# Kernel tuning notes

Hardware: AMD Instinct MI355X
Metric: run time of the kernel (lower is better)

## Reference

```python
import jax, jax.numpy as jnp
import numpy as np

B, K, V = 8192, 1024, 2


def setup_inputs() -> dict:
    key = jax.random.key(0)
    k1, k2, k3, k4, k5, k6 = jax.random.split(key, 6)
    z = jax.random.normal(k1, (B, K), dtype=jnp.float32)
    # -1 means no intervention for that sample
    intervention_target = jax.random.randint(k2, (B,), -1, K)
    intervention_variant = jax.random.randint(k3, (B,), 0, V)
    raw_adjacency = jax.random.normal(k4, (K, K), dtype=jnp.float32) * 0.05
    intervention_means = jax.random.normal(k5, (K, V), dtype=jnp.float32)
    intervention_log_scales = jax.random.normal(k6, (K, V), dtype=jnp.float32) * 0.1
    return {
        "z": z,
        "intervention_target": intervention_target,
        "intervention_variant": intervention_variant,
        "raw_adjacency": raw_adjacency,
        "intervention_means": intervention_means,
        "intervention_log_scales": intervention_log_scales,
    }


def _scm_forward(z, target, variant, raw_adjacency, means, log_scales):
    Kd = z.shape[1]
    # strictly-lower-triangular adjacency (row j holds parents of node j)
    A = raw_adjacency * jnp.tril(jnp.ones((Kd, Kd), z.dtype), k=-1)

    def step(u, xs):
        a_row, mean_row, logsc_row, z_j, j = xs
        # forward substitution: u_j = z_j + sum_{i<j} A[j,i] * u_i
        # columns >= j of u are still zero and A row is zero there too
        value = z_j + u @ a_row  # [B]
        # intervention overwrite for samples with target == j
        m = mean_row[variant]                 # [B]
        s = jnp.exp(logsc_row[variant])       # [B]
        value = jnp.where(target == j, m + s * z_j, value)
        u = jax.lax.dynamic_update_slice(u, value[:, None], (0, j))
        return u, None

    u0 = jnp.zeros_like(z)
    xs = (A, means, log_scales, z.T, jnp.arange(Kd))
    u, _ = jax.lax.scan(step, u0, xs)
    return u


def reference(z, intervention_target, intervention_variant, raw_adjacency,
              intervention_means, intervention_log_scales):
    return _scm_forward(z, intervention_target, intervention_variant,
                        raw_adjacency, intervention_means, intervention_log_scales)
```

## Files before the change

### kernel.cpp

```cpp
#include <hip/hip_runtime.h>
#include <hip/hip_bf16.h>
#include <cstdint>

#define KDIM 1024
#define BDIM 8192
#define VDIM 2
#define NBLK 16

typedef __attribute__((ext_vector_type(8))) short short8;
typedef __attribute__((ext_vector_type(4))) float f32x4;

__device__ inline unsigned short f2bf(float x) {
  unsigned u = __builtin_bit_cast(unsigned, x);
  u = (u + 0x7FFFu + ((u >> 16) & 1u)) >> 16;
  return (unsigned short)u;
}

__device__ inline float bf2f(unsigned short x) {
  return __builtin_bit_cast(float, (unsigned)x << 16);
}


#define STAGE_T(DST, SRC, ROW0, COL0, LD)                                   \
  {                                                                         \
    const float* _s = (SRC);                                                \
    _Pragma("unroll") for (int _p = 0; _p < 4; ++_p) {                      \
      const int _m = _p * 16 + rw;                                          \
      float4 _v = *(const float4*)(_s + (size_t)((ROW0) + _m) * (LD) +      \
                                   (COL0) + 4 * k4);                        \
      (DST)[4 * k4 + 0][_m] = _v.x;                                         \
      (DST)[4 * k4 + 1][_m] = _v.y;                                         \
      (DST)[4 * k4 + 2][_m] = _v.z;                                         \
      (DST)[4 * k4 + 3][_m] = _v.w;                                         \
    }                                                                       \
  }

#define STAGE_D(DST, SRC, ROW0, COL0, LD)                                   \
  {                                                                         \
    const float* _s = (SRC);                                                \
    _Pragma("unroll") for (int _p = 0; _p < 4; ++_p) {                      \
      const int _kk = _p * 16 + rw;                                         \
      *(float4*)&(DST)[_kk][4 * k4] =                                       \
          *(const float4*)(_s + (size_t)((ROW0) + _kk) * (LD) + (COL0) +    \
                           4 * k4);                                         \
    }                                                                       \
  }

#define ZERO_ACC                                                            \
  _Pragma("unroll") for (int _a = 0; _a < 4; ++_a)                          \
      _Pragma("unroll") for (int _b = 0; _b < 4; ++_b) acc[_a][_b] = 0.f;

__device__ __forceinline__ void mac64(const float (*Ls)[68],
                                      const float (*Rs)[68], int tm, int tn,
                                      float acc[4][4]) {
#pragma unroll 4
  for (int k = 0; k < 64; ++k) {
    const float4 av = *(const float4*)&Ls[k][4 * tm];
    const float4 bv = *(const float4*)&Rs[k][4 * tn];
    const float aa[4] = {av.x, av.y, av.z, av.w};
    const float bb4[4] = {bv.x, bv.y, bv.z, bv.w};
#pragma unroll
    for (int a = 0; a < 4; ++a)
#pragma unroll
      for (int b = 0; b < 4; ++b) acc[a][b] += aa[a] * bb4[b];
  }
}

#define STORE_MT(R0, C0)                                                    \
  _Pragma("unroll") for (int _a = 0; _a < 4; ++_a) {                        \
    *(float4*)(MT + (size_t)((R0) + 4 * tm + _a) * KDIM + (C0) + 4 * tn) =  \
        make_float4(acc[_a][0], acc[_a][1], acc[_a][2], acc[_a][3]);        \
  }

#define MBF_TILE(R0, C0, BUF)                                               \
  {                                                                         \
    __syncthreads();                                                        \
    _Pragma("unroll") for (int _a = 0; _a < 4; ++_a)                        \
        _Pragma("unroll") for (int _b = 0; _b < 4; ++_b)                    \
            (BUF)[4 * tm + _a][4 * tn + _b] = acc[_a][_b];                  \
    __syncthreads();                                                        \
    const int _tr = tid >> 4, _tc = tid & 15;                               \
    _Pragma("unroll") for (int _p = 0; _p < 4; ++_p) {                      \
      const int _il = _p * 16 + _tr;                                        \
      ushort4 _o;                                                           \
      _o.x = f2bf((BUF)[4 * _tc + 0][_il]);                                 \
      _o.y = f2bf((BUF)[4 * _tc + 1][_il]);                                 \
      _o.z = f2bf((BUF)[4 * _tc + 2][_il]);                                 \
      _o.w = f2bf((BUF)[4 * _tc + 3][_il]);                                 \
      *(ushort4*)(Mbf + (size_t)((C0) + _il) * KDIM + (R0) + 4 * _tc) = _o; \
    }                                                                       \
  }

__global__ __launch_bounds__(256) void prep_inv(const float* __restrict__ A,
                                                float* __restrict__ MT,
                                                unsigned short* __restrict__ Mbf) {
  __shared__ float As[64 * 64];
  const int base = blockIdx.x * 64;
  for (int i = threadIdx.x; i < 64 * 64; i += 256)
    As[i] = A[(size_t)(base + (i >> 6)) * KDIM + base + (i & 63)];
  __syncthreads();
  if (threadIdx.x < 64) {
    const int c = threadIdx.x;
    float m[64];
#pragma unroll
    for (int r = 0; r < 64; ++r) m[r] = (r == c) ? 1.f : 0.f;
#pragma unroll
    for (int r = 1; r < 64; ++r) {
      float acc0 = 0.f, acc1 = 0.f;
#pragma unroll
      for (int i = 0; i < 64; ++i) {
        if (i >= r) break;
        if (i & 1) acc1 += As[r * 64 + i] * m[i];
        else       acc0 += As[r * 64 + i] * m[i];
      }
      const float v = acc0 + acc1;
      m[r] = (r > c) ? v : m[r];
    }
#pragma unroll
    for (int r = 0; r < 64; r += 4) {
      float4 v = make_float4(m[r], m[r + 1], m[r + 2], m[r + 3]);
      *(float4*)(MT + (size_t)(base + c) * KDIM + base + r) = v;
    }
#pragma unroll
    for (int r = 0; r < 64; ++r)
      Mbf[(size_t)(base + r) * KDIM + base + c] = f2bf(m[r]);
  }
}

__global__ __launch_bounds__(256) void comb01(const float* __restrict__ A,
                                              float* __restrict__ MT,
                                              unsigned short* __restrict__ Mbf) {
  int b = blockIdx.x;
  const int rt = b & 1;
  const int jt = (b >> 1) & 1;
  const int s = b >> 2;
  const int base = s * 256;

  __shared__ float Ls[64][68];
  __shared__ float Rs[64][68];
  __shared__ float tQ0L[64][68];
  __shared__ float tQ0H[64][68];
  __shared__ float tP0[64][68];
  __shared__ float tP1[64][68];

  const int tid = threadIdx.x;
  const int k4 = tid & 15;
  const int rw = tid >> 4;
  const int tm = tid >> 4;
  const int tn = tid & 15;
  float acc[4][4];

  if (jt == 0) {
    STAGE_T(Ls, MT, base, base, KDIM);
    STAGE_T(Rs, A, base + 64, base, KDIM);
    __syncthreads();
    ZERO_ACC;
    mac64(Ls, Rs, tm, tn, acc);
    __syncthreads();
#pragma unroll
    for (int a = 0; a < 4; ++a)
#pragma unroll
      for (int b2 = 0; b2 < 4; ++b2) tP0[4 * tn + b2][4 * tm + a] = acc[a][b2];
    STAGE_D(Rs, MT, base + 64, base + 64, KDIM);
    __syncthreads();
    ZERO_ACC;
    mac64(tP0, Rs, tm, tn, acc);
    __syncthreads();
#pragma unroll
    for (int a = 0; a < 4; ++a)
#pragma unroll
      for (int b2 = 0; b2 < 4; ++b2) tQ0L[4 * tn + b2][4 * tm + a] = acc[a][b2];
    if (rt == 0) {
      STORE_MT(base, base + 64);
      MBF_TILE(base, base + 64, Rs);
    }
  }
  __syncthreads();

  if (rt == 1) {
    STAGE_T(Ls, MT, base + 128, base + 128, KDIM);
    STAGE_T(Rs, A, base + 192, base + 128, KDIM);
    __syncthreads();
    ZERO_ACC;
    mac64(Ls, Rs, tm, tn, acc);
    __syncthreads();
#pragma unroll
    for (int a = 0; a < 4; ++a)
#pragma unroll
      for (int b2 = 0; b2 < 4; ++b2) tP1[4 * tn + b2][4 * tm + a] = acc[a][b2];
    STAGE_D(Rs, MT, base + 192, base + 192, KDIM);
    __syncthreads();
    ZERO_ACC;
    mac64(tP1, Rs, tm, tn, acc);
    __syncthreads();
#pragma unroll
    for (int a = 0; a < 4; ++a)
#pragma unroll
      for (int b2 = 0; b2 < 4; ++b2) tQ0H[4 * tm + a][4 * tn + b2] = acc[a][b2];
    if (jt == 1) {
      STORE_MT(base + 128, base + 192);
      MBF_TILE(base + 128, base + 192, Rs);
    }
  }
  __syncthreads();

  STAGE_T(Ls, MT, base + 64 * jt, base + 64 * jt, KDIM);
  __syncthreads();
  for (int kb2 = 0; kb2 <= rt; ++kb2) {
    ZERO_ACC;
    for (int kb = jt; kb < 2; ++kb) {
      STAGE_T(Rs, A, base + 128 + 64 * kb2, base + 64 * kb, KDIM);
      __syncthreads();
      mac64(kb == jt ? Ls : tQ0L, Rs, tm, tn, acc);
      __syncthreads();
    }
    if (kb2 == 0) {
#pragma unroll
      for (int a = 0; a < 4; ++a)
#pragma unroll
        for (int b2 = 0; b2 < 4; ++b2) tP0[4 * tn + b2][4 * tm + a] = acc[a][b2];
    } else {
#pragma unroll
      for (int a = 0; a < 4; ++a)
#pragma unroll
        for (int b2 = 0; b2 < 4; ++b2) tP1[4 * tn + b2][4 * tm + a] = acc[a][b2];
    }
  }
  __syncthreads();

  ZERO_ACC;
  if (rt == 0) {
    STAGE_D(Rs, MT, base + 128, base + 128, KDIM);
    __syncthreads();
    mac64(tP0, Rs, tm, tn, acc);
    __syncthreads();
  } else {
    mac64(tP0, tQ0H, tm, tn, acc);
    __syncthreads();
    STAGE_D(Rs, MT, base + 192, base + 192, KDIM);
    __syncthreads();
    mac64(tP1, Rs, tm, tn, acc);
    __syncthreads();
  }
  STORE_MT(base + 64 * jt, base + 128 + 64 * rt);
  MBF_TILE(base + 64 * jt, base + 128 + 64 * rt, Rs);
}

__global__ __launch_bounds__(256) void p4_stream(
    const float* __restrict__ A, float* __restrict__ MT,
    float* __restrict__ Pt, const float* __restrict__ Z,
    unsigned short* __restrict__ Zbf, unsigned short* __restrict__ Mbf,
    int do_zbf) {
  __shared__ float Ls[64][68];
  __shared__ float Rs[64][68];

  if (blockIdx.x >= 32) {
    const int wid = blockIdx.x - 32;
    const int nw = gridDim.x - 32;
    const int idx0 = wid * 256 + threadIdx.x;
    const int stride = nw * 256;
    const float4 z4 = make_float4(0.f, 0.f, 0.f, 0.f);
    const uint4 u4 = make_uint4(0u, 0u, 0u, 0u);

    for (int i = idx0; i < 256 * 1024; i += stride) {
      const int blk = i >> 10, off = i & 1023;
      const int bi = blk >> 4, bj = blk & 15;
      if (bi <= bj) continue;
      *(float4*)(MT + (size_t)(bi * 64 + (off >> 4)) * KDIM + bj * 64 +
                 4 * (off & 15)) = z4;
    }
    for (int i = idx0; i < 256 * 512; i += stride) {
      const int blk = i >> 9, off = i & 511;
      const int bi = blk >> 4, bj = blk & 15;
      if (bi >= bj) continue;
      *(uint4*)(Mbf + (size_t)(bi * 64 + (off >> 3)) * KDIM + bj * 64 +
                8 * (off & 7)) = u4;
    }
    if (do_zbf) {
      for (int i = idx0; i < BDIM * KDIM / 4; i += stride) {
        float4 v = *(const float4*)(Z + 4 * (size_t)i);
        ushort4 o;
        o.x = f2bf(v.x);
        o.y = f2bf(v.y);
        o.z = f2bf(v.z);
        o.w = f2bf(v.w);
        *(ushort4*)(Zbf + 4 * (size_t)i) = o;
      }
    }
    return;
  }

  int b = blockIdx.x;
  const int T = 4;
  const int rb = b % T; b /= T;
  const int jb = b % T; b /= T;
  const int c = b;
  const int h = 64 * T;
  const int base = c * 2 * h;

  const int tid = threadIdx.x;
  const int k4 = tid & 15;
  const int rw = tid >> 4;
  const int tm = tid >> 4;
  const int tn = tid & 15;
  float acc[4][4];
  ZERO_ACC;

  for (int kb = jb; kb < T; ++kb) {
    STAGE_T(Ls, MT, base + 64 * jb, base + 64 * kb, KDIM);
    STAGE_T(Rs, A, base + h + 64 * rb, base + 64 * kb, KDIM);
    __syncthreads();
    mac64(Ls, Rs, tm, tn, acc);
    __syncthreads();
  }

  float* P0 = Pt + (size_t)c * h * h;
#pragma unroll
  for (int a = 0; a < 4; ++a)
    *(float4*)(P0 + (size_t)(64 * jb + 4 * tm + a) * h + 64 * rb + 4 * tn) =
        make_float4(acc[a][0], acc[a][1], acc[a][2], acc[a][3]);
}

template <int T>
__global__ __launch_bounds__(256) void p_k(const float* __restrict__ A,
                                           const float* __restrict__ MT,
                                           float* __restrict__ Pt) {
  int b = blockIdx.x;
  const int rb = b % T; b /= T;
  const int jb = b % T; b /= T;
  const int c = b;
  const int h = 64 * T;
  const int base = c * 2 * h;

  __shared__ float Ls[64][68];
  __shared__ float Rs[64][68];
  const int tid = threadIdx.x;
  const int k4 = tid & 15;
  const int rw = tid >> 4;
  const int tm = tid >> 4;
  const int tn = tid & 15;
  float acc[4][4];
  ZERO_ACC;

  for (int kb = jb; kb < T; ++kb) {
    STAGE_T(Ls, MT, base + 64 * jb, base + 64 * kb, KDIM);
    STAGE_T(Rs, A, base + h + 64 * rb, base + 64 * kb, KDIM);
    __syncthreads();
    mac64(Ls, Rs, tm, tn, acc);
    __syncthreads();
  }

  float* P0 = Pt + (size_t)c * h * h;
#pragma unroll
  for (int a = 0; a < 4; ++a)
    *(float4*)(P0 + (size_t)(64 * jb + 4 * tm + a) * h + 64 * rb + 4 * tn) =
        make_float4(acc[a][0], acc[a][1], acc[a][2], acc[a][3]);
}

template <int T>
__global__ __launch_bounds__(256) void q_k(float* __restrict__ MT,
                                           const float* __restrict__ Pt,
                                           unsigned short* __restrict__ Mbf) {
  int b = blockIdx.x;
  const int rb = b % T; b /= T;
  const int jb = b % T; b /= T;
  const int c = b;
  const int h = 64 * T;
  const int base = c * 2 * h;

  __shared__ float Ls[64][68];
  __shared__ float Rs[64][68];
  const int tid = threadIdx.x;
  const int k4 = tid & 15;
  const int rw = tid >> 4;
  const int tm = tid >> 4;
  const int tn = tid & 15;
  float acc[4][4];
  ZERO_ACC;

  const float* P0 = Pt + (size_t)c * h * h;
  for (int kb = 0; kb <= rb; ++kb) {
    STAGE_T(Ls, P0, 64 * jb, 64 * kb, h);
    STAGE_D(Rs, MT, base + h + 64 * kb, base + h + 64 * rb, KDIM);
    __syncthreads();
    mac64(Ls, Rs, tm, tn, acc);
    __syncthreads();
  }

  STORE_MT(base + 64 * jb, base + h + 64 * rb);
  MBF_TILE(base + 64 * jb, base + h + 64 * rb, Ls);
}

#define LDB 72

template <int ZBF>
__global__ __launch_bounds__(256) void gemm_mfma(
    const float* __restrict__ Z, const unsigned short* __restrict__ Zbf,
    const unsigned short* __restrict__ Mbf, const float* __restrict__ MT,
    const int* __restrict__ tgt, const int* __restrict__ var,
    const float* __restrict__ means, const float* __restrict__ lsc,
    float* __restrict__ C) {
  __shared__ unsigned short As[128][LDB];
  __shared__ unsigned short Bs[128][LDB];
  __shared__ float scoef[128];
  __shared__ int stb[128];

  const int d = blockIdx.x;
  const int xbl = d & 7;
  const int nir = (d >> 3) & 7;
  const int xbh = d >> 6;
  const int xb = xbh * 8 + xbl;
  const int ni = (xb & 32) ? (7 - nir) : nir;
  const int b0 = xb * 128;
  const int i0 = ni * 128;

  const int tid = threadIdx.x;
  const int w = tid >> 6;
  const int lane = tid & 63;
  const int wr = w >> 1, wc = w & 1;
  const int mlane = lane & 15;
  const int q = lane >> 4;

  const int rq = tid >> 4, kq = tid & 15;
  const int cb = tid >> 3, ck = tid & 7;

  f32x4 acc[4][4];
#pragma unroll
  for (int a = 0; a < 4; ++a)
#pragma unroll
    for (int b = 0; b < 4; ++b) acc[a][b] = (f32x4){0.f, 0.f, 0.f, 0.f};

  const int nkb = 2 * (ni + 1);
  for (int kb = 0; kb < nkb; ++kb) {
    const int k0 = kb * 64;
    if (ZBF) {
#pragma unroll
      for (int p = 0; p < 4; ++p) {
        const int r = p * 32 + cb;
        *(uint4*)&As[r][8 * ck] =
            *(const uint4*)(Zbf + (size_t)(b0 + r) * KDIM + k0 + 8 * ck);
      }
    } else {
#pragma unroll
      for (int p = 0; p < 8; ++p) {
        const int r = p * 16 + rq;
        float4 zv = *(const float4*)(Z + (size_t)(b0 + r) * KDIM + k0 + 4 * kq);
        ushort4 o;
        o.x = f2bf(zv.x);
        o.y = f2bf(zv.y);
        o.z = f2bf(zv.z);
        o.w = f2bf(zv.w);
        *(ushort4*)&As[r][4 * kq] = o;
      }
    }
#pragma unroll
    for (int p = 0; p < 4; ++p) {
      const int c = p * 32 + cb;
      *(uint4*)&Bs[c][8 * ck] =
          *(const uint4*)(Mbf + (size_t)(i0 + c) * KDIM + k0 + 8 * ck);
    }
    __syncthreads();
#pragma unroll
    for (int ks = 0; ks < 2; ++ks) {
      const int kf = ks * 32 + q * 8;
      short8 av[4], bv[4];
#pragma unroll
      for (int a = 0; a < 4; ++a)
        av[a] = *(const short8*)&As[wr * 64 + 16 * a + mlane][kf];
#pragma unroll
      for (int b = 0; b < 4; ++b)
        bv[b] = *(const short8*)&Bs[wc * 64 + 16 * b + mlane][kf];
#pragma unroll
      for (int a = 0; a < 4; ++a)
#pragma unroll
        for (int b = 0; b < 4; ++b)
          acc[a][b] =
              __builtin_amdgcn_mfma_f32_16x16x32_bf16(av[a], bv[b], acc[a][b], 0, 0, 0);
    }
    __syncthreads();
  }

  {
    const int s = tid >> 1, h2 = tid & 1;
    const int br = b0 + s;
    const int tb = tgt[br];
    float part = 0.f;
    if (tb >= 0) {
      const int nk16 = (tb >> 4) + 1;
      if (ZBF) {
        const unsigned short* zr = Zbf + (size_t)br * KDIM;
        const unsigned short* mr = Mbf + (size_t)tb * KDIM;
        for (int c16 = h2; c16 < nk16; c16 += 2) {
          const uint4 za = *(const uint4*)(zr + c16 * 16);
          const uint4 zb2 = *(const uint4*)(zr + c16 * 16 + 8);
          const uint4 ma = *(const uint4*)(mr + c16 * 16);
          const uint4 mb2 = *(const uint4*)(mr + c16 * 16 + 8);
          const unsigned zw[8] = {za.x, za.y, za.z, za.w,
                                  zb2.x, zb2.y, zb2.z, zb2.w};
          const unsigned mw[8] = {ma.x, ma.y, ma.z, ma.w,
                                  mb2.x, mb2.y, mb2.z, mb2.w};
#pragma unroll
          for (int wv = 0; wv < 8; ++wv) {
            part += __builtin_bit_cast(float, zw[wv] << 16) *
                    __builtin_bit_cast(float, mw[wv] << 16);
            part += __builtin_bit_cast(float, zw[wv] & 0xFFFF0000u) *
                    __builtin_bit_cast(float, mw[wv] & 0xFFFF0000u);
          }
        }
      } else {
        const float* zr = Z + (size_t)br * KDIM;
        const unsigned short* mr = Mbf + (size_t)tb * KDIM;
        const int nk8 = (tb >> 3) + 1;
        for (int c8 = h2; c8 < nk8; c8 += 2) {
          const float4 z0 = *(const float4*)(zr + c8 * 8);
          const float4 z1 = *(const float4*)(zr + c8 * 8 + 4);
          const ushort4 m0 = *(const ushort4*)(mr + c8 * 8);
          const ushort4 m1 = *(const ushort4*)(mr + c8 * 8 + 4);
          part += z0.x * bf2f(m0.x) + z0.y * bf2f(m0.y) + z0.z * bf2f(m0.z) +
                  z0.w * bf2f(m0.w) + z1.x * bf2f(m1.x) + z1.y * bf2f(m1.y) +
                  z1.z * bf2f(m1.z) + z1.w * bf2f(m1.w);
        }
      }
    }
    part += __shfl_down(part, 1);
    if (h2 == 0) {
      float cf = 0.f;
      int tbs = 0;
      if (tb >= 0) {
        const int v = var[br];
        const float mval = means[tb * VDIM + v];
        const float sval = expf(lsc[tb * VDIM + v]);
        const float zv = Z[(size_t)br * KDIM + tb];
        cf = (mval + sval * zv) - part;
        tbs = tb;
      }
      scoef[s] = cf;
      stb[s] = tbs;
    }
  }
  __syncthreads();

#pragma unroll
  for (int a = 0; a < 4; ++a) {
    const int l0 = wr * 64 + 16 * a + q * 4;
    const int row0 = b0 + l0;
#pragma unroll
    for (int b = 0; b < 4; ++b) {
      const int col = i0 + wc * 64 + 16 * b + mlane;
      float* Cp = C + (size_t)row0 * KDIM + col;
#pragma unroll
      for (int j = 0; j < 4; ++j) {
        const float cf = scoef[l0 + j];
        const float corr = cf * MT[(size_t)stb[l0 + j] * KDIM + col];
        Cp[j * KDIM] = acc[a][b][j] + corr;
      }
    }
  }
}

extern "C" void kernel_launch(void* const* d_in, const int* in_sizes, int n_in,
                              void* d_out, int out_size, void* d_ws,
                              size_t ws_size, hipStream_t stream) {
  const float* z = (const float*)d_in[0];
  const int* tgt = (const int*)d_in[1];
  const int* var = (const int*)d_in[2];
  const float* A = (const float*)d_in[3];
  const float* means = (const float*)d_in[4];
  const float* lsc = (const float*)d_in[5];
  float* out = (float*)d_out;

  char* ws = (char*)d_ws;
  float* MT = (float*)ws;
  unsigned short* Mbf = (unsigned short*)(ws + (4u << 20));
  float* Pt2 = (float*)(ws + (6u << 20));
  float* Pt3 = (float*)(ws + (6u << 20) + (512u << 10));
  unsigned short* Zbf = (unsigned short*)(ws + (7u << 20) + (512u << 10));
  const int use_zbf =
      ws_size >= (7u << 20) + (512u << 10) + (size_t)BDIM * KDIM * 2 ? 1 : 0;

  hipLaunchKernelGGL(prep_inv, dim3(NBLK), dim3(256), 0, stream, A, MT, Mbf);
  hipLaunchKernelGGL(comb01, dim3(16), dim3(256), 0, stream, A, MT, Mbf);
  hipLaunchKernelGGL(p4_stream, dim3(512), dim3(256), 0, stream, A, MT, Pt2, z,
                     Zbf, Mbf, use_zbf);
  hipLaunchKernelGGL((q_k<4>), dim3(32), dim3(256), 0, stream, MT, Pt2, Mbf);
  hipLaunchKernelGGL((p_k<8>), dim3(64), dim3(256), 0, stream, A, MT, Pt3);
  hipLaunchKernelGGL((q_k<8>), dim3(64), dim3(256), 0, stream, MT, Pt3, Mbf);
  if (use_zbf)
    hipLaunchKernelGGL((gemm_mfma<1>), dim3((BDIM / 128) * (KDIM / 128)),
                       dim3(256), 0, stream, z, Zbf, Mbf, MT, tgt, var, means,
                       lsc, out);
  else
    hipLaunchKernelGGL((gemm_mfma<0>), dim3((BDIM / 128) * (KDIM / 128)),
                       dim3(256), 0, stream, z, Zbf, Mbf, MT, tgt, var, means,
                       lsc, out);
}
```

Before: 256.5 us.

## Fuse diagonal-block inversion into comb01 and load B tiles via global_load_lds

Drops the separate prep_inv launch. Each comb01 block now inverts its four 64x64 diagonal blocks itself, using the shared-memory pool, before combining them, which removes one kernel launch and its serialization. Every comb01 block repeats this inversion redundantly and writes MT, while only one block per group writes Mbf, so identical values are written concurrently. In the GEMM, the Mbf B-tile is loaded straight into LDS with global_load_lds in an XOR-swizzled layout instead of going through registers, which may cut VGPR traffic and bank conflicts.

```diff
diff --git a/kernel.cpp b/kernel.cpp
--- a/kernel.cpp
+++ b/kernel.cpp
@@ -6,6 +6,15 @@
 #define BDIM 8192
 #define VDIM 2
 #define NBLK 16
+
+#if defined(__has_builtin)
+#if __has_builtin(__builtin_amdgcn_global_load_lds)
+#define HAS_GLL 1
+#endif
+#endif
+#ifndef HAS_GLL
+#define HAS_GLL 0
+#endif
 
 typedef __attribute__((ext_vector_type(8))) short short8;
 typedef __attribute__((ext_vector_type(4))) float f32x4;
@@ -91,42 +100,6 @@
     }                                                                       \
   }
 
-__global__ __launch_bounds__(256) void prep_inv(const float* __restrict__ A,
-                                                float* __restrict__ MT,
-                                                unsigned short* __restrict__ Mbf) {
-  __shared__ float As[64 * 64];
-  const int base = blockIdx.x * 64;
-  for (int i = threadIdx.x; i < 64 * 64; i += 256)
-    As[i] = A[(size_t)(base + (i >> 6)) * KDIM + base + (i & 63)];
-  __syncthreads();
-  if (threadIdx.x < 64) {
-    const int c = threadIdx.x;
-    float m[64];
-#pragma unroll
-    for (int r = 0; r < 64; ++r) m[r] = (r == c) ? 1.f : 0.f;
-#pragma unroll
-    for (int r = 1; r < 64; ++r) {
-      float acc0 = 0.f, acc1 = 0.f;
-#pragma unroll
-      for (int i = 0; i < 64; ++i) {
-        if (i >= r) break;
-        if (i & 1) acc1 += As[r * 64 + i] * m[i];
-        else       acc0 += As[r * 64 + i] * m[i];
-      }
-      const float v = acc0 + acc1;
-      m[r] = (r > c) ? v : m[r];
-    }
-#pragma unroll
-    for (int r = 0; r < 64; r += 4) {
-      float4 v = make_float4(m[r], m[r + 1], m[r + 2], m[r + 3]);
-      *(float4*)(MT + (size_t)(base + c) * KDIM + base + r) = v;
-    }
-#pragma unroll
-    for (int r = 0; r < 64; ++r)
-      Mbf[(size_t)(base + r) * KDIM + base + c] = f2bf(m[r]);
-  }
-}
-
 __global__ __launch_bounds__(256) void comb01(const float* __restrict__ A,
                                               float* __restrict__ MT,
                                               unsigned short* __restrict__ Mbf) {
@@ -136,12 +109,14 @@
   const int s = b >> 2;
   const int base = s * 256;
 
-  __shared__ float Ls[64][68];
-  __shared__ float Rs[64][68];
-  __shared__ float tQ0L[64][68];
-  __shared__ float tQ0H[64][68];
-  __shared__ float tP0[64][68];
-  __shared__ float tP1[64][68];
+  __shared__ float shpool[6 * 64 * 68];
+  float (*Ls)[68] = (float(*)[68])(shpool);
+  float (*Rs)[68] = (float(*)[68])(shpool + 4352);
+  float (*tQ0L)[68] = (float(*)[68])(shpool + 2 * 4352);
+  float (*tQ0H)[68] = (float(*)[68])(shpool + 3 * 4352);
+  float (*tP0)[68] = (float(*)[68])(shpool + 4 * 4352);
+  float (*tP1)[68] = (float(*)[68])(shpool + 5 * 4352);
+  float* As4 = shpool + 2 * 4352;
 
   const int tid = threadIdx.x;
   const int k4 = tid & 15;
@@ -149,6 +124,41 @@
   const int tm = tid >> 4;
   const int tn = tid & 15;
   float acc[4][4];
+
+  {
+    const int g = tid >> 6;
+    const int c = tid & 63;
+    const int dbase = base + g * 64;
+    float* Asg = As4 + g * 4096;
+    for (int r = 0; r < 64; ++r)
+      Asg[r * 64 + c] = A[(size_t)(dbase + r) * KDIM + dbase + c];
+    __syncthreads();
+    float m[64];
+#pragma unroll
+    for (int r = 0; r < 64; ++r) m[r] = (r == c) ? 1.f : 0.f;
+#pragma unroll
+    for (int r = 1; r < 64; ++r) {
+      float a0 = 0.f, a1 = 0.f;
+#pragma unroll
+      for (int i = 0; i < 64; ++i) {
+        if (i >= r) break;
+        if (i & 1) a1 += Asg[r * 64 + i] * m[i];
+        else       a0 += Asg[r * 64 + i] * m[i];
+      }
+      const float v = a0 + a1;
+      m[r] = (r > c) ? v : m[r];
+    }
+#pragma unroll
+    for (int r = 0; r < 64; r += 4)
+      *(float4*)(MT + (size_t)(dbase + c) * KDIM + dbase + r) =
+          make_float4(m[r], m[r + 1], m[r + 2], m[r + 3]);
+    if (jt == 0 && rt == 0) {
+#pragma unroll
+      for (int r = 0; r < 64; ++r)
+        Mbf[(size_t)(dbase + r) * KDIM + dbase + c] = f2bf(m[r]);
+    }
+    __syncthreads();
+  }
 
   if (jt == 0) {
     STAGE_T(Ls, MT, base, base, KDIM);
@@ -401,7 +411,11 @@
     const float* __restrict__ means, const float* __restrict__ lsc,
     float* __restrict__ C) {
   __shared__ unsigned short As[128][LDB];
+#if HAS_GLL
+  __shared__ unsigned short Bs[128][64];
+#else
   __shared__ unsigned short Bs[128][LDB];
+#endif
   __shared__ float scoef[128];
   __shared__ int stb[128];
 
@@ -453,12 +467,30 @@
         *(ushort4*)&As[r][4 * kq] = o;
       }
     }
+#if HAS_GLL
+    {
+      const int rl = lane >> 3;
+      const int ch = lane & 7;
+#pragma unroll
+      for (int i = 0; i < 4; ++i) {
+        const int row = w * 32 + i * 8 + rl;
+        const int sch = ch ^ (row & 7);
+        const unsigned short* src =
+            Mbf + (size_t)(i0 + row) * KDIM + k0 + sch * 8;
+        __builtin_amdgcn_global_load_lds(
+            (const __attribute__((address_space(1))) void*)src,
+            (__attribute__((address_space(3))) void*)&Bs[w * 32 + i * 8][0],
+            16, 0, 0);
+      }
+    }
+#else
 #pragma unroll
     for (int p = 0; p < 4; ++p) {
       const int c = p * 32 + cb;
       *(uint4*)&Bs[c][8 * ck] =
           *(const uint4*)(Mbf + (size_t)(i0 + c) * KDIM + k0 + 8 * ck);
     }
+#endif
     __syncthreads();
 #pragma unroll
     for (int ks = 0; ks < 2; ++ks) {
@@ -467,9 +499,19 @@
 #pragma unroll
       for (int a = 0; a < 4; ++a)
         av[a] = *(const short8*)&As[wr * 64 + 16 * a + mlane][kf];
+#if HAS_GLL
+      const char* BsB = (const char*)&Bs[0][0];
+#pragma unroll
+      for (int b = 0; b < 4; ++b) {
+        const int row = wc * 64 + 16 * b + mlane;
+        bv[b] = *(const short8*)(BsB + row * 128 +
+                                 ((2 * kf) ^ ((row & 7) << 4)));
+      }
+#else
 #pragma unroll
       for (int b = 0; b < 4; ++b)
         bv[b] = *(const short8*)&Bs[wc * 64 + 16 * b + mlane][kf];
+#endif
 #pragma unroll
       for (int a = 0; a < 4; ++a)
 #pragma unroll
@@ -578,7 +620,6 @@
   const int use_zbf =
       ws_size >= (7u << 20) + (512u << 10) + (size_t)BDIM * KDIM * 2 ? 1 : 0;
 
-  hipLaunchKernelGGL(prep_inv, dim3(NBLK), dim3(256), 0, stream, A, MT, Mbf);
   hipLaunchKernelGGL(comb01, dim3(16), dim3(256), 0, stream, A, MT, Mbf);
   hipLaunchKernelGGL(p4_stream, dim3(512), dim3(256), 0, stream, A, MT, Pt2, z,
                      Zbf, Mbf, use_zbf);
```

After: 244.1 us. -4.8%, faster.
